# Performance work log

Hardware: AMD Instinct MI355X
Metric: run time of the kernel (lower is better)

The kernel has to match this reference:

```python
import jax, jax.numpy as jnp
import numpy as np
import math

B, S, D = 4, 2048, 1024
H, KV = 16, 4
HD = D // H
GROUPS = H // KV

def _alibi_slopes(n):
    # n assumed power of 2 here (n=16)
    start = 2.0 ** (-2.0 ** (-(math.log2(n) - 3)))
    return np.array([start * start ** i for i in range(n)], dtype=np.float32)

def setup_inputs() -> dict:
    key = jax.random.key(0)
    ks = jax.random.split(key, 5)
    sc = 0.02
    return {
        "x": jax.random.normal(ks[0], (B, S, D), jnp.float32),
        "Wq": jax.random.normal(ks[1], (D, H * HD), jnp.float32) * sc,
        "Wk": jax.random.normal(ks[2], (D, KV * HD), jnp.float32) * sc,
        "Wv": jax.random.normal(ks[3], (D, KV * HD), jnp.float32) * sc,
        "Wo": jax.random.normal(ks[4], (H * HD, D), jnp.float32) * sc,
    }

def reference(x, Wq, Wk, Wv, Wo):
    b, s, _ = x.shape
    scale = HD ** -0.5
    q = (x @ Wq).reshape(b, s, H, HD).transpose(0, 2, 1, 3)   # [b,H,s,hd]
    k = (x @ Wk).reshape(b, s, KV, HD).transpose(0, 2, 1, 3)  # [b,KV,s,hd]
    v = (x @ Wv).reshape(b, s, KV, HD).transpose(0, 2, 1, 3)
    k = jnp.repeat(k, GROUPS, axis=1)  # [b,H,s,hd]
    v = jnp.repeat(v, GROUPS, axis=1)
    attn = jnp.einsum('bhqd,bhkd->bhqk', q, k) * scale
    # ALiBi bias: slope_h * (j - i)
    slopes = jnp.asarray(_alibi_slopes(H))
    pos = jnp.arange(s, dtype=jnp.float32)
    rel = pos[None, :] - pos[:, None]                     # [s,s]
    attn = attn + slopes[None, :, None, None] * rel[None, None, :, :]
    attn = jax.nn.softmax(attn, axis=-1)
    out = jnp.einsum('bhqk,bhkd->bhqd', attn, v)
    out = out.transpose(0, 2, 1, 3).reshape(b, s, H * HD)
    return out @ Wo
```

## Files before the change

### kernel.cpp

```cpp
#include <hip/hip_runtime.h>

typedef unsigned short u16;
typedef unsigned int u32;
typedef unsigned char u8;
typedef _Float16 f16;
typedef __attribute__((ext_vector_type(8))) f16 f16x8;
typedef __attribute__((ext_vector_type(4))) float f32x4;

#define S_LEN 2048
#define DM 1024
#define QKVW 1536
#define KVSTRIDE (S_LEN * 64)

__device__ __forceinline__ u16 f2h(float x) {
    f16 h = (f16)x;
    return __builtin_bit_cast(u16, h);
}

__device__ __forceinline__ void g2l16(const void* g, void* l) {
    __builtin_amdgcn_global_load_lds((const __attribute__((address_space(1))) u32*)g,
                                     (__attribute__((address_space(3))) u32*)l, 16, 0, 0);
}

__global__ __launch_bounds__(256)
void prep(const float* __restrict__ x, u16* __restrict__ xh,
          const float* __restrict__ Wq, const float* __restrict__ Wk,
          const float* __restrict__ Wv, const float* __restrict__ Wo,
          u16* __restrict__ Wtq, u16* __restrict__ Wto) {
    __shared__ float tbuf[32][33];
    const int tid = threadIdx.x;
    const int blk = blockIdx.x;
    if (blk < 8192) {
        int i = blk * 256 + tid;
        float4 v = ((const float4*)x)[i];
        ((ushort4*)xh)[i] = make_ushort4(f2h(v.x), f2h(v.y), f2h(v.z), f2h(v.w));
        return;
    }
    int t = blk - 8192;
    const float* src;
    u16* dst;
    int C, cx, ry;
    if (t < 1024)      { src = Wq; dst = Wtq;               C = 1024; cx = t & 31; ry = t >> 5; }
    else if (t < 1280) { t -= 1024; src = Wk; dst = Wtq + 1024 * 1024; C = 256; cx = t & 7; ry = t >> 3; }
    else if (t < 1536) { t -= 1280; src = Wv; dst = Wtq + 1280 * 1024; C = 256; cx = t & 7; ry = t >> 3; }
    else               { t -= 1536; src = Wo; dst = Wto;    C = 1024; cx = t & 31; ry = t >> 5; }
    const int c0 = cx * 32, r0 = ry * 32;
    const int tx = tid & 31, ty = tid >> 5;
#pragma unroll
    for (int i = 0; i < 4; ++i)
        tbuf[ty + 8 * i][tx] = src[(long)(r0 + ty + 8 * i) * C + c0 + tx];
    __syncthreads();
#pragma unroll
    for (int i = 0; i < 4; ++i)
        dst[(long)(c0 + ty + 8 * i) * 1024 + r0 + tx] = f2h(tbuf[tx][ty + 8 * i]);
}

template <bool FUSED>
__global__ __launch_bounds__(256, 3)
void gemm_bt(const u16* __restrict__ A, const u16* __restrict__ Bt,
             float* __restrict__ Cf, u16* __restrict__ Qp,
             u16* __restrict__ Kp, u16* __restrict__ Vp, int N, int K) {
    __shared__ __attribute__((aligned(16))) u16 sA[128 * 32];
    __shared__ __attribute__((aligned(16))) u16 sB[128 * 32];
    const int tid = threadIdx.x, w = tid >> 6, lane = tid & 63;
    const int quad = lane >> 4, l15 = lane & 15;
    const int wm = w & 1, wn = w >> 1;
    const long row0 = (long)blockIdx.x * 128, col0 = (long)blockIdx.y * 128;

    f32x4 acc[4][4];
#pragma unroll
    for (int mb = 0; mb < 4; ++mb)
#pragma unroll
        for (int nb = 0; nb < 4; ++nb) acc[mb][nb] = (f32x4){0.f, 0.f, 0.f, 0.f};

    const int r = lane >> 2;
    const int cch = (lane & 3) ^ (r & 3);

    for (int kt = 0; kt < K; kt += 32) {
        __syncthreads();
#pragma unroll
        for (int i = 0; i < 4; ++i) {
            int gid = w + 4 * i;
            int buf = gid >> 3, seg = gid & 7;
            const u16* src = buf ? Bt : A;
            long base0 = buf ? col0 : row0;
            const u16* g = src + (base0 + seg * 16 + r) * (long)K + kt + cch * 8;
            u16* dst = (buf ? sB : sA) + seg * 512;
            g2l16(g, dst);
        }
        __syncthreads();

        f16x8 bfr[4];
#pragma unroll
        for (int nb = 0; nb < 4; ++nb) {
            int rr = wn * 64 + nb * 16 + l15;
            bfr[nb] = *(const f16x8*)(sB + rr * 32 + ((quad ^ (l15 & 3)) * 8));
        }
#pragma unroll
        for (int mb = 0; mb < 4; ++mb) {
            int rr = wm * 64 + mb * 16 + l15;
            f16x8 af = *(const f16x8*)(sA + rr * 32 + ((quad ^ (l15 & 3)) * 8));
#pragma unroll
            for (int nb = 0; nb < 4; ++nb)
                acc[mb][nb] = __builtin_amdgcn_mfma_f32_16x16x32_f16(af, bfr[nb], acc[mb][nb], 0, 0, 0);
        }
    }

    if constexpr (FUSED) {
        const int bq = (int)(row0 >> 11);
        u16* kpbat = Kp + (long)bq * 4 * KVSTRIDE;
        u16* vpbat = Vp + (long)bq * 4 * KVSTRIDE;
#pragma unroll
        for (int mb = 0; mb < 4; ++mb) {
            const int key0 = ((int)(row0 & 2047)) + wm * 64 + mb * 16 + quad * 4;
#pragma unroll
            for (int nb = 0; nb < 4; ++nb) {
                const int colbase = (int)col0 + wn * 64 + nb * 16;
                if (colbase < 1024) {
#pragma unroll
                    for (int rr = 0; rr < 4; ++rr) {
                        long row = row0 + wm * 64 + mb * 16 + quad * 4 + rr;
                        Qp[row * 1024 + colbase + l15] = f2h(acc[mb][nb][rr]);
                    }
                } else if (colbase < 1280) {
                    const int cc = colbase - 1024;
                    const int d = (cc & 63) + l15;
                    u16* kp = kpbat + (long)(cc >> 6) * KVSTRIDE;
                    const int dpart = (d >> 5) * 512 + ((d >> 3) & 3) * 128 + (d & 7);
#pragma unroll
                    for (int rr = 0; rr < 4; ++rr) {
                        int key = key0 + rr;
                        kp[(key >> 4) * 1024 + (key & 15) * 8 + dpart] = f2h(acc[mb][nb][rr]);
                    }
                } else {
                    const int cc = colbase - 1280;
                    const int d = (cc & 63) + l15;
                    u16* vp = vpbat + (long)(cc >> 6) * KVSTRIDE;
                    const long idx = (long)((key0 >> 5) * 4 + (d >> 4)) * 512 +
                                     ((key0 >> 3) & 3) * 128 + (d & 15) * 8 + (key0 & 7);
                    ushort4 pk = make_ushort4(f2h(acc[mb][nb][0]), f2h(acc[mb][nb][1]),
                                              f2h(acc[mb][nb][2]), f2h(acc[mb][nb][3]));
                    *(ushort4*)(vp + idx) = pk;
                }
            }
        }
    } else {
#pragma unroll
        for (int mb = 0; mb < 4; ++mb)
#pragma unroll
            for (int nb = 0; nb < 4; ++nb)
#pragma unroll
                for (int rr = 0; rr < 4; ++rr) {
                    long row = row0 + wm * 64 + mb * 16 + quad * 4 + rr;
                    long col = col0 + wn * 64 + nb * 16 + l15;
                    Cf[row * N + col] = acc[mb][nb][rr];
                }
    }
}

__device__ const u8 UH[21]  = {15,15,14,14,13,13,12,10,12,11,11, 9, 8, 7, 6, 5, 4, 3, 2, 1, 0};
__device__ const u8 UK0[21] = { 0,16, 0,16, 0,16, 1,16,17,10,21,21,24,26,28,29,30,30,31,31,31};
__device__ const u8 UK1[21] = {16,32,16,32,16,32,17,32,32,21,32,32,32,32,32,32,32,32,32,32,32};
__device__ const u8 UC[21]  = { 0, 1, 0, 1, 0, 1, 0, 0, 1, 0, 1, 0, 0, 0, 0, 0, 0, 0, 0, 0, 0};

__global__ __launch_bounds__(256, 4)
void attn(const u16* __restrict__ Qp, const u16* __restrict__ Kp,
          const u16* __restrict__ Vp, u16* __restrict__ Oh,
          float* __restrict__ Of, float* __restrict__ Ls) {
    __shared__ __attribute__((aligned(16))) u16 sP[2][4][16][72];
    const int tid = threadIdx.x, w = tid >> 6, lane = tid & 63;
    const int quad = lane >> 4, l15 = lane & 15;

    const int id = blockIdx.x;
    const int u = id >> 6, s = id & 63;
    const int b = s >> 4, qt = s & 15;
    const int h = UH[u];
    const int kt0 = UK0[u], kt1 = UK1[u];
    const int chunk = UC[u];
    const bool split = (u <= 10) && (u != 7);
    const int kvh = h >> 2;

    const float c1 = 0.125f * 1.44269504f;
    const float c2 = __builtin_amdgcn_exp2f(-0.5f * (float)(h + 1)) * 1.44269504f;
    const float d0 = -8.0f - c2 * 2047.0f;

    const long qrow0 = (long)b * S_LEN + qt * 128 + w * 32;

    f16x8 qf[2][2];
#pragma unroll
    for (int rg = 0; rg < 2; ++rg)
#pragma unroll
        for (int ch = 0; ch < 2; ++ch)
            qf[rg][ch] = *(const f16x8*)(Qp + (qrow0 + rg * 16 + l15) * 1024 +
                                         h * 64 + ch * 32 + quad * 8);

    const f16x8 vone = {(f16)1.f, (f16)1.f, (f16)1.f, (f16)1.f,
                        (f16)1.f, (f16)1.f, (f16)1.f, (f16)1.f};

    f32x4 oacc[2][4];
    f32x4 lacc[2];
#pragma unroll
    for (int rg = 0; rg < 2; ++rg) {
#pragma unroll
        for (int nb = 0; nb < 4; ++nb) oacc[rg][nb] = (f32x4){0.f, 0.f, 0.f, 0.f};
        lacc[rg] = (f32x4){0.f, 0.f, 0.f, 0.f};
    }

    const u16* kpb = Kp + (long)(b * 4 + kvh) * KVSTRIDE + lane * 8;
    const u16* vpb = Vp + (long)(b * 4 + kvh) * KVSTRIDE + lane * 8;

    for (int kt = kt0; kt < kt1; ++kt) {
        __builtin_amdgcn_s_barrier();
        f16x8 kf[8];
#pragma unroll
        for (int j = 0; j < 8; ++j)
            kf[j] = *(const f16x8*)(kpb + (long)(kt * 8 + j) * 512);
        const float kcb = fmaf(c2, (float)(kt * 64 + l15), d0);
#pragma unroll
        for (int rg = 0; rg < 2; ++rg) {
#pragma unroll
            for (int kb = 0; kb < 4; ++kb) {
                f32x4 z = (f32x4){0.f, 0.f, 0.f, 0.f};
                __builtin_amdgcn_s_setprio(1);
                z = __builtin_amdgcn_mfma_f32_16x16x32_f16(qf[rg][0], kf[2 * kb], z, 0, 0, 0);
                z = __builtin_amdgcn_mfma_f32_16x16x32_f16(qf[rg][1], kf[2 * kb + 1], z, 0, 0, 0);
                __builtin_amdgcn_s_setprio(0);
                float kc = fmaf(c2, (float)(16 * kb), kcb);
#pragma unroll
                for (int rr = 0; rr < 4; ++rr) {
                    float p = __builtin_amdgcn_exp2f(fmaf(z[rr], c1, kc));
                    sP[rg][w][quad * 4 + rr][kb * 16 + l15] = f2h(p);
                }
            }
        }
        f16x8 vf[8];
#pragma unroll
        for (int j = 0; j < 8; ++j)
            vf[j] = *(const f16x8*)(vpb + (long)(kt * 8 + j) * 512);
#pragma unroll
        for (int rg = 0; rg < 2; ++rg)
#pragma unroll
            for (int ch = 0; ch < 2; ++ch) {
                f16x8 pf = *(const f16x8*)(&sP[rg][w][l15][ch * 32 + quad * 8]);
                __builtin_amdgcn_s_setprio(1);
#pragma unroll
                for (int nb = 0; nb < 4; ++nb)
                    oacc[rg][nb] = __builtin_amdgcn_mfma_f32_16x16x32_f16(pf, vf[ch * 4 + nb],
                                                                          oacc[rg][nb], 0, 0, 0);
                lacc[rg] = __builtin_amdgcn_mfma_f32_16x16x32_f16(pf, vone, lacc[rg], 0, 0, 0);
                __builtin_amdgcn_s_setprio(0);
            }
    }

#pragma unroll
    for (int rg = 0; rg < 2; ++rg) {
        if (split) {
            const int hs = h - 11;
#pragma unroll
            for (int rr = 0; rr < 4; ++rr) {
                long rowg = qrow0 + rg * 16 + quad * 4 + rr;
                if (l15 == 0)
                    Ls[(long)(chunk * 8192) * 5 + rowg * 5 + hs] = lacc[rg][rr];
#pragma unroll
                for (int nb = 0; nb < 4; ++nb)
                    Of[((long)(chunk * 8192) + rowg) * 320 + hs * 64 + nb * 16 + l15] =
                        oacc[rg][nb][rr];
            }
        } else {
#pragma unroll
            for (int rr = 0; rr < 4; ++rr) {
                const float linv = 1.0f / lacc[rg][rr];
#pragma unroll
                for (int nb = 0; nb < 4; ++nb) {
                    long row = qrow0 + rg * 16 + quad * 4 + rr;
                    long col = h * 64 + nb * 16 + l15;
                    Oh[row * DM + col] = f2h(oacc[rg][nb][rr] * linv);
                }
            }
        }
    }
}

__global__ __launch_bounds__(256)
void norm_split(const float* __restrict__ Of, const float* __restrict__ Ls,
                u16* __restrict__ Oh) {
    const int gid = blockIdx.x * 256 + threadIdx.x;
    const int d4 = gid & 15;
    const int rh = gid >> 4;
    const int hs = rh % 5;
    const int row = rh / 5;
    const float l = Ls[rh] + Ls[rh + 40960];
    const float4 a = ((const float4*)Of)[rh * 16 + d4];
    const float4 bq = ((const float4*)Of)[(rh + 40960) * 16 + d4];
    const float inv = 1.0f / l;
    const int col = (hs + 11) * 64 + d4 * 4;
    ((ushort4*)(Oh + (long)row * DM + col))[0] =
        make_ushort4(f2h((a.x + bq.x) * inv), f2h((a.y + bq.y) * inv),
                     f2h((a.z + bq.z) * inv), f2h((a.w + bq.w) * inv));
}

extern "C" void kernel_launch(void* const* d_in, const int* in_sizes, int n_in,
                              void* d_out, int out_size, void* d_ws, size_t ws_size,
                              hipStream_t stream) {
    const float* x = (const float*)d_in[0];
    const float* Wq = (const float*)d_in[1];
    const float* Wk = (const float*)d_in[2];
    const float* Wv = (const float*)d_in[3];
    const float* Wo = (const float*)d_in[4];
    char* ws = (char*)d_ws;
    const size_t MB = 1 << 20;

    u16* xh = (u16*)ws;
    u16* Wtq = (u16*)(ws + 16 * MB);
    u16* Wto = (u16*)(ws + 19 * MB);
    u16* Qp = (u16*)(ws + 21 * MB);
    u16* Kp = (u16*)(ws + 37 * MB);
    u16* Vp = (u16*)(ws + 41 * MB);
    u16* Oh = xh;

    float* Of = (float*)d_out;
    float* Ls = Of + 2 * 8192 * 5 * 64;

    prep<<<10752, 256, 0, stream>>>(x, xh, Wq, Wk, Wv, Wo, Wtq, Wto);
    gemm_bt<true><<<dim3(64, 12), 256, 0, stream>>>(xh, Wtq, nullptr, Qp, Kp, Vp, QKVW, 1024);
    attn<<<1344, 256, 0, stream>>>(Qp, Kp, Vp, Oh, Of, Ls);
    norm_split<<<2560, 256, 0, stream>>>(Of, Ls, Oh);
    gemm_bt<false><<<dim3(64, 8), 256, 0, stream>>>(Oh, Wto, (float*)d_out, nullptr, nullptr, nullptr, 1024, 1024);
}
```

Baseline: 199.8 us.

## Double GEMM K-step to 64 and prefetch next K tile in attention loop

The GEMM now stages a 64-wide K slice per iteration, loading two 32-wide halves into doubled LDS buffers. This halves the number of barrier pairs per K sweep, at the cost of more LDS per block, which may reduce occupancy under launch_bounds(256,3). The attention loop now loads the first K tile before the loop. Each iteration issues all QK MFMAs first, then prefetches the next K tile's registers so those global loads overlap the exp/softmax work. This keeps more live registers.

```diff
diff --git a/kernel.cpp b/kernel.cpp
--- a/kernel.cpp
+++ b/kernel.cpp
@@ -60,8 +60,8 @@
 void gemm_bt(const u16* __restrict__ A, const u16* __restrict__ Bt,
              float* __restrict__ Cf, u16* __restrict__ Qp,
              u16* __restrict__ Kp, u16* __restrict__ Vp, int N, int K) {
-    __shared__ __attribute__((aligned(16))) u16 sA[128 * 32];
-    __shared__ __attribute__((aligned(16))) u16 sB[128 * 32];
+    __shared__ __attribute__((aligned(16))) u16 sA[2 * 128 * 32];
+    __shared__ __attribute__((aligned(16))) u16 sB[2 * 128 * 32];
     const int tid = threadIdx.x, w = tid >> 6, lane = tid & 63;
     const int quad = lane >> 4, l15 = lane & 15;
     const int wm = w & 1, wn = w >> 1;
@@ -76,33 +76,38 @@
     const int r = lane >> 2;
     const int cch = (lane & 3) ^ (r & 3);
 
-    for (int kt = 0; kt < K; kt += 32) {
+    for (int kt = 0; kt < K; kt += 64) {
         __syncthreads();
 #pragma unroll
-        for (int i = 0; i < 4; ++i) {
+        for (int i = 0; i < 8; ++i) {
             int gid = w + 4 * i;
-            int buf = gid >> 3, seg = gid & 7;
+            int buf = gid >> 4, kh = (gid >> 3) & 1, seg = gid & 7;
             const u16* src = buf ? Bt : A;
             long base0 = buf ? col0 : row0;
-            const u16* g = src + (base0 + seg * 16 + r) * (long)K + kt + cch * 8;
-            u16* dst = (buf ? sB : sA) + seg * 512;
+            const u16* g = src + (base0 + seg * 16 + r) * (long)K + kt + kh * 32 + cch * 8;
+            u16* dst = (buf ? sB : sA) + kh * 4096 + seg * 512;
             g2l16(g, dst);
         }
         __syncthreads();
 
-        f16x8 bfr[4];
-#pragma unroll
-        for (int nb = 0; nb < 4; ++nb) {
-            int rr = wn * 64 + nb * 16 + l15;
-            bfr[nb] = *(const f16x8*)(sB + rr * 32 + ((quad ^ (l15 & 3)) * 8));
-        }
+        f16x8 bfr[2][4];
+#pragma unroll
+        for (int kh = 0; kh < 2; ++kh)
+#pragma unroll
+            for (int nb = 0; nb < 4; ++nb) {
+                int rr = wn * 64 + nb * 16 + l15;
+                bfr[kh][nb] = *(const f16x8*)(sB + kh * 4096 + rr * 32 + ((quad ^ (l15 & 3)) * 8));
+            }
 #pragma unroll
         for (int mb = 0; mb < 4; ++mb) {
             int rr = wm * 64 + mb * 16 + l15;
-            f16x8 af = *(const f16x8*)(sA + rr * 32 + ((quad ^ (l15 & 3)) * 8));
-#pragma unroll
-            for (int nb = 0; nb < 4; ++nb)
-                acc[mb][nb] = __builtin_amdgcn_mfma_f32_16x16x32_f16(af, bfr[nb], acc[mb][nb], 0, 0, 0);
+#pragma unroll
+            for (int kh = 0; kh < 2; ++kh) {
+                f16x8 af = *(const f16x8*)(sA + kh * 4096 + rr * 32 + ((quad ^ (l15 & 3)) * 8));
+#pragma unroll
+                for (int nb = 0; nb < 4; ++nb)
+                    acc[mb][nb] = __builtin_amdgcn_mfma_f32_16x16x32_f16(af, bfr[kh][nb], acc[mb][nb], 0, 0, 0);
+            }
         }
     }
 
@@ -209,30 +214,45 @@
     const u16* kpb = Kp + (long)(b * 4 + kvh) * KVSTRIDE + lane * 8;
     const u16* vpb = Vp + (long)(b * 4 + kvh) * KVSTRIDE + lane * 8;
 
+    f16x8 kf[8];
+#pragma unroll
+    for (int j = 0; j < 8; ++j)
+        kf[j] = *(const f16x8*)(kpb + (long)(kt0 * 8 + j) * 512);
+
     for (int kt = kt0; kt < kt1; ++kt) {
         __builtin_amdgcn_s_barrier();
-        f16x8 kf[8];
+
+        f32x4 z[2][4];
+        __builtin_amdgcn_s_setprio(1);
+#pragma unroll
+        for (int rg = 0; rg < 2; ++rg)
+#pragma unroll
+            for (int kb = 0; kb < 4; ++kb) {
+                f32x4 zz = (f32x4){0.f, 0.f, 0.f, 0.f};
+                zz = __builtin_amdgcn_mfma_f32_16x16x32_f16(qf[rg][0], kf[2 * kb], zz, 0, 0, 0);
+                zz = __builtin_amdgcn_mfma_f32_16x16x32_f16(qf[rg][1], kf[2 * kb + 1], zz, 0, 0, 0);
+                z[rg][kb] = zz;
+            }
+        __builtin_amdgcn_s_setprio(0);
+
+        const int ktn = (kt + 1 < kt1) ? kt + 1 : kt;
 #pragma unroll
         for (int j = 0; j < 8; ++j)
-            kf[j] = *(const f16x8*)(kpb + (long)(kt * 8 + j) * 512);
+            kf[j] = *(const f16x8*)(kpb + (long)(ktn * 8 + j) * 512);
+
         const float kcb = fmaf(c2, (float)(kt * 64 + l15), d0);
 #pragma unroll
-        for (int rg = 0; rg < 2; ++rg) {
+        for (int rg = 0; rg < 2; ++rg)
 #pragma unroll
             for (int kb = 0; kb < 4; ++kb) {
-                f32x4 z = (f32x4){0.f, 0.f, 0.f, 0.f};
-                __builtin_amdgcn_s_setprio(1);
-                z = __builtin_amdgcn_mfma_f32_16x16x32_f16(qf[rg][0], kf[2 * kb], z, 0, 0, 0);
-                z = __builtin_amdgcn_mfma_f32_16x16x32_f16(qf[rg][1], kf[2 * kb + 1], z, 0, 0, 0);
-                __builtin_amdgcn_s_setprio(0);
                 float kc = fmaf(c2, (float)(16 * kb), kcb);
 #pragma unroll
                 for (int rr = 0; rr < 4; ++rr) {
-                    float p = __builtin_amdgcn_exp2f(fmaf(z[rr], c1, kc));
+                    float p = __builtin_amdgcn_exp2f(fmaf(z[rg][kb][rr], c1, kc));
                     sP[rg][w][quad * 4 + rr][kb * 16 + l15] = f2h(p);
                 }
             }
-        }
+
         f16x8 vf[8];
 #pragma unroll
         for (int j = 0; j < 8; ++j)
```

New measurement: 213.4 us. 1.07x slower.
